# Optimization experiments

Measured on AMD Instinct MI355X. Metric: run time of the kernel, lower is better.

## Reference

```python
import jax, jax.numpy as jnp
import numpy as np

K = 7          # kernel_size
STRIDE = 1
GC = 4         # group_channels (fixed in module)
BN_EPS = 1e-5


def setup_inputs() -> dict:
    key = jax.random.key(0)
    ks = jax.random.split(key, 4)
    B, C, H, W = 4, 256, 56, 56
    Cr = C // 4              # reduction_ratio = 4
    G = C // GC              # groups = 64
    K2 = K * K               # 49
    x = jax.random.normal(ks[0], (B, C, H, W), jnp.float32)
    w1 = jax.random.normal(ks[1], (Cr, C), jnp.float32) * 0.05   # conv1 1x1
    b1 = jnp.zeros((Cr,), jnp.float32)
    gamma = jnp.ones((Cr,), jnp.float32)
    beta = jnp.zeros((Cr,), jnp.float32)
    bn_mean = jnp.zeros((Cr,), jnp.float32)
    bn_var = jnp.ones((Cr,), jnp.float32)
    w2 = jax.random.normal(ks[2], (K2 * G, Cr), jnp.float32) * 0.05  # conv2 1x1
    b2 = jnp.zeros((K2 * G,), jnp.float32)
    return {"x": x, "w1": w1, "b1": b1, "gamma": gamma, "beta": beta,
            "bn_mean": bn_mean, "bn_var": bn_var, "w2": w2, "b2": b2}


def reference(x, w1, b1, gamma, beta, bn_mean, bn_var, w2, b2):
    B, C, H, W = x.shape
    G = C // GC
    K2 = K * K
    p = (K - 1) // 2

    # kernel-generation branch (stride == 1 -> no avgpool)
    y = jnp.einsum('oc,bchw->bohw', w1, x) + b1[None, :, None, None]
    # BatchNorm (inference, running stats)
    inv = gamma / jnp.sqrt(bn_var + BN_EPS)
    y = y * inv[None, :, None, None] + (beta - bn_mean * inv)[None, :, None, None]
    y = jax.nn.relu(y)
    weight = jnp.einsum('oc,bchw->bohw', w2, y) + b2[None, :, None, None]
    Ho, Wo = weight.shape[2], weight.shape[3]
    weight = weight.reshape(B, G, K2, Ho, Wo)

    # unfold: zero-pad then gather k*k shifted views (channel-major like torch Unfold)
    xp = jnp.pad(x, ((0, 0), (0, 0), (p, p), (p, p)))
    patches = jnp.stack(
        [xp[:, :, i:i + H:STRIDE, j:j + W:STRIDE] for i in range(K) for j in range(K)],
        axis=2)                                    # (B, C, K2, Ho, Wo)
    patches = patches.reshape(B, G, GC, K2, Ho, Wo)

    # per-pixel dynamic kernel multiply-accumulate over k^2
    out = jnp.einsum('bgkhw,bgckhw->bgchw', weight, patches)
    return out.reshape(B, C, Ho, Wo)
```

## Files before the change

kernel.cpp:

```cpp
#include <hip/hip_runtime.h>
#include <hip/hip_fp16.h>

typedef _Float16 h8 __attribute__((ext_vector_type(8)));
typedef _Float16 h2v __attribute__((ext_vector_type(2)));
typedef __fp16 fp16x2 __attribute__((ext_vector_type(2)));
typedef float f32x4 __attribute__((ext_vector_type(4)));

#define HW 3136
#define NPX 12544
#define YSTR 96
#define XROW 14
#define XSEG 116
#define PS2 456
#define WGT_W 3648

union UH { unsigned int u; h2v h; fp16x2 p; };
__device__ __forceinline__ h2v uh(unsigned int u) { UH v; v.u = u; return v.h; }
__device__ __forceinline__ unsigned int hu(h2v h) { UH v; v.h = h; return v.u; }
#define BLO(w) __builtin_shufflevector(w, w, 0, 0)
#define BHI(w) __builtin_shufflevector(w, w, 1, 1)

__device__ __forceinline__ unsigned int pkrtz(float a, float b) {
    UH v; v.p = __builtin_amdgcn_cvt_pkrtz(a, b); return v.u;
}
__device__ __forceinline__ unsigned short f2hu(float f) {
    union { __half h; unsigned short u; } v; v.h = __float2half(f); return v.u;
}
__device__ __forceinline__ float fget(const float4& v, int e) {
    return e == 0 ? v.x : e == 1 ? v.y : e == 2 ? v.z : v.w;
}

__global__ __launch_bounds__(256) void kyw(
    const float* __restrict__ x, const float* __restrict__ w1,
    const float* __restrict__ b1, const float* __restrict__ gamma,
    const float* __restrict__ beta, const float* __restrict__ mean,
    const float* __restrict__ var, const float* __restrict__ w2,
    const float* __restrict__ b2, unsigned short* __restrict__ ytb,
    unsigned short* __restrict__ w2b96)
{
    __shared__ unsigned short xt[64 * 264];
    const int t = threadIdx.x, bid = blockIdx.x;

    if (bid >= 196) {
        const int r0 = (bid - 196) * 16;
#pragma unroll
        for (int i = 0; i < 6; ++i) {
            int j = i * 256 + t;
            int row = r0 + j / 96, col = j - (j / 96) * 96;
            int c8 = row / 448, rem = row - c8 * 448;
            int g = rem / 56, s = rem - g * 56;
            int ki = s >> 3, kj = s & 7;
            float v = 0.f;
            if (kj < 7) {
                int o = (c8 * 8 + g) * 49 + ki * 7 + kj;
                v = col < 64 ? w2[o * 64 + col] : (col == 64 ? b2[o] : 0.f);
            }
            w2b96[row * 96 + col] = f2hu(v);
        }
        return;
    }

    const int px0 = bid * 64;
    const int b = px0 / HW;
    const int p0 = px0 - b * HW;

    {
        unsigned int* xw = (unsigned int*)xt;
#pragma unroll
        for (int s = 0; s < 4; ++s)
#pragma unroll
            for (int i = 0; i < 2; ++i) {
                int j = i * 256 + t;
                int cp2 = j >> 2, pq = j & 3;
                const float* s0 = x + (size_t)(b * 256 + cp2 * 2) * HW
                                    + p0 + s * 16 + pq * 4;
                float4 v0 = *(const float4*)(s0);
                float4 v1 = *(const float4*)(s0 + HW);
                int pxb = s * 16 + pq * 4;
                xw[(pxb + 0) * 132 + cp2] = pkrtz(v0.x, v1.x);
                xw[(pxb + 1) * 132 + cp2] = pkrtz(v0.y, v1.y);
                xw[(pxb + 2) * 132 + cp2] = pkrtz(v0.z, v1.z);
                xw[(pxb + 3) * 132 + cp2] = pkrtz(v0.w, v1.w);
            }
    }
    if (t < 64) {
        unsigned short* yr = ytb + (size_t)(px0 + t) * YSTR + 64;
        ushort4 one; one.x = 0x3C00u; one.y = 0; one.z = 0; one.w = 0;
        ushort4 z; z.x = 0; z.y = 0; z.z = 0; z.w = 0;
        *(ushort4*)(yr) = one;
#pragma unroll
        for (int q = 1; q < 8; ++q) *(ushort4*)(yr + q * 4) = z;
    }
    __syncthreads();

    const int lane = t & 63, wave = t >> 6;
    const int n = lane & 15, quad = lane >> 4;
    const int m0 = wave * 16;

    h8 A[8];
#pragma unroll
    for (int k = 0; k < 8; ++k) {
        const float* wrow = w1 + (m0 + n) * 256 + k * 32 + quad * 8;
        float4 wa = *(const float4*)(wrow);
        float4 wb = *(const float4*)(wrow + 4);
        union { uint4 u; h8 h; } Au;
        Au.u.x = pkrtz(wa.x, wa.y);
        Au.u.y = pkrtz(wa.z, wa.w);
        Au.u.z = pkrtz(wb.x, wb.y);
        Au.u.w = pkrtz(wb.z, wb.w);
        A[k] = Au.h;
    }
    float sc[4], sh[4];
#pragma unroll
    for (int r = 0; r < 4; ++r) {
        int m = m0 + quad * 4 + r;
        sc[r] = gamma[m] * rsqrtf(var[m] + 1e-5f);
        sh[r] = beta[m] - mean[m] * sc[r] + b1[m] * sc[r];
    }

#pragma unroll
    for (int s = 0; s < 4; ++s) {
        f32x4 acc = {0.f, 0.f, 0.f, 0.f};
#pragma unroll
        for (int k = 0; k < 8; ++k) {
            h8 bv = *(const h8*)(&xt[(s * 16 + n) * 264 + k * 32 + quad * 8]);
            acc = __builtin_amdgcn_mfma_f32_16x16x32_f16(A[k], bv, acc, 0, 0, 0);
        }
        uint2 pk;
        pk.x = pkrtz(fmaxf(acc[0] * sc[0] + sh[0], 0.f),
                     fmaxf(acc[1] * sc[1] + sh[1], 0.f));
        pk.y = pkrtz(fmaxf(acc[2] * sc[2] + sh[2], 0.f),
                     fmaxf(acc[3] * sc[3] + sh[3], 0.f));
        *(uint2*)(ytb + (size_t)(px0 + s * 16 + n) * YSTR + m0 + quad * 4) = pk;
    }
}

__global__ __launch_bounds__(256, 7) void kmain(
    const float* __restrict__ x, const unsigned short* __restrict__ w2b96,
    const unsigned short* __restrict__ ytb, float* __restrict__ out)
{
    __shared__ __align__(16) unsigned int smem_u[WGT_W + 16 * XSEG];
    unsigned short* wgt16 = (unsigned short*)smem_u;
    unsigned int* xsb = smem_u + WGT_W;

    const int t = threadIdx.x;
    const int pix = t & 15, sub = t >> 4;
    const int lane = t & 63, wave = t >> 6;
    const int bc = blockIdx.x;
    const int b = bc >> 3, c8 = bc & 7;
    const int w0 = blockIdx.y * 8, h0 = blockIdx.z * 2;
    const int ph = pix >> 3, pw = pix & 7;
    const int h = h0 + ph, w = w0 + pw;
    const int n = lane & 15, quad = lane >> 4;

    const int Pn = b * HW + (h0 + (n >> 3)) * 56 + w0 + (n & 7);
    const unsigned short* yrp = ytb + (size_t)Pn * YSTR + quad * 8;
    const h8 bf0 = *(const h8*)(yrp);
    const h8 bf1 = *(const h8*)(yrp + 32);
    const h8 bf2 = *(const h8*)(yrp + 64);

    if (t < 128) {
        const int seg = t & 15, jr = t >> 4;
        const int jg = seg >> 1, jcp = seg & 1;
        const int hh = h0 + jr - 3;
        const bool rowok = (hh >= 0) && (hh < 56);
        const float* src = x + ((size_t)b * 256 + c8 * 32 + jg * 4 + jcp * 2) * HW + hh * 56;
        float4 va[2][4];
#pragma unroll
        for (int q = 0; q < 4; ++q) {
            int col0 = w0 - 4 + q * 4;
            bool ok = rowok && (col0 >= 0) && (col0 <= 52);
#pragma unroll
            for (int ci = 0; ci < 2; ++ci)
                va[ci][q] = ok ? *(const float4*)(src + ci * HW + col0)
                              : make_float4(0.f, 0.f, 0.f, 0.f);
        }
        unsigned int* dst = xsb + seg * XSEG + jr * XROW;
#pragma unroll
        for (int q = 0; q < 4; ++q)
#pragma unroll
            for (int e = 0; e < 4; ++e) {
                int c = q * 4 + e - 1;
                if (c >= 0 && c < 14)
                    dst[c] = pkrtz(fget(va[0][q], e), fget(va[1][q], e));
            }
    }

    {
        const int c0 = c8 * 448;
        for (int tile = wave; tile < 28; tile += 4) {
            const unsigned short* ap = w2b96 + (size_t)(c0 + tile * 16 + n) * 96 + quad * 8;
            h8 af0 = *(const h8*)(ap);
            h8 af1 = *(const h8*)(ap + 32);
            h8 af2 = *(const h8*)(ap + 64);
            f32x4 acc = {0.f, 0.f, 0.f, 0.f};
            acc = __builtin_amdgcn_mfma_f32_16x16x32_f16(af0, bf0, acc, 0, 0, 0);
            acc = __builtin_amdgcn_mfma_f32_16x16x32_f16(af1, bf1, acc, 0, 0, 0);
            acc = __builtin_amdgcn_mfma_f32_16x16x32_f16(af2, bf2, acc, 0, 0, 0);
            uint2 pk2;
            pk2.x = pkrtz(acc[0], acc[1]);
            pk2.y = pkrtz(acc[2], acc[3]);
            *(uint2*)(wgt16 + n * PS2 + tile * 16 + quad * 4) = pk2;
        }
    }
    __syncthreads();

    const int g = sub & 7, cp = sub >> 3;
    const unsigned short* wr16 = wgt16 + pix * PS2 + g * 56;
    const unsigned int* xr = xsb + (g * 2 + cp) * XSEG + ph * XROW + pw;
    h2v acA = {(_Float16)0.f, (_Float16)0.f};
    h2v acB = acA;
#pragma unroll
    for (int ki = 0; ki < 7; ++ki) {
        uint4 wq = *(const uint4*)(wr16 + ki * 8);
        const unsigned int* xrow = xr + ki * XROW;
        unsigned int xv[7];
#pragma unroll
        for (int j = 0; j < 7; ++j) xv[j] = xrow[j];
        h2v w01 = uh(wq.x), w23 = uh(wq.y), w45 = uh(wq.z), w6p = uh(wq.w);
        acA += BLO(w01) * uh(xv[0]);
        acB += BHI(w01) * uh(xv[1]);
        acA += BLO(w23) * uh(xv[2]);
        acB += BHI(w23) * uh(xv[3]);
        acA += BLO(w45) * uh(xv[4]);
        acB += BHI(w45) * uh(xv[5]);
        acA += BLO(w6p) * uh(xv[6]);
    }
    h2v acc2 = acA + acB;
    float a0 = (float)acc2[0];
    float a1 = (float)acc2[1];

    size_t ob = ((size_t)b * 256 + c8 * 32 + g * 4 + cp * 2) * HW + h * 56 + w;
    out[ob] = a0;
    out[ob + HW] = a1;
}

extern "C" void kernel_launch(void* const* d_in, const int* in_sizes, int n_in,
                              void* d_out, int out_size, void* d_ws, size_t ws_size,
                              hipStream_t stream) {
    const float* x     = (const float*)d_in[0];
    const float* w1    = (const float*)d_in[1];
    const float* b1    = (const float*)d_in[2];
    const float* gamma = (const float*)d_in[3];
    const float* beta  = (const float*)d_in[4];
    const float* mean  = (const float*)d_in[5];
    const float* var   = (const float*)d_in[6];
    const float* w2    = (const float*)d_in[7];
    const float* b2    = (const float*)d_in[8];
    float* out = (float*)d_out;

    unsigned short* ytb   = (unsigned short*)d_ws;
    unsigned short* w2b96 = ytb + (size_t)NPX * YSTR;
    hipLaunchKernelGGL(kyw, dim3(420), dim3(256), 0, stream,
                       x, w1, b1, gamma, beta, mean, var, w2, b2, ytb, w2b96);
    hipLaunchKernelGGL(kmain, dim3(32, 7, 28), dim3(256), 0, stream,
                       x, w2b96, ytb, out);
}
```

Baseline: 133.9 us.

## Process four output rows per block in kmain to reuse weight tiles and input halo

Each kmain block now covers a 4x8 pixel tile instead of 2x8, halving the grid along H. The w2 A-fragments loaded per tile feed two MFMA chains (for two 16-pixel groups), and the x halo (10 rows instead of 8) is staged once for both row pairs. The intent is to cut redundant w2 global loads and halo reloads. In exchange it doubles shared memory for generated weights, lowers occupancy to 4 blocks/SM, and raises register pressure.

Measured after the change: 121.7 us. 9.1% less time.

```diff
diff --git a/kernel.cpp b/kernel.cpp
--- a/kernel.cpp
+++ b/kernel.cpp
@@ -10,9 +10,9 @@
 #define NPX 12544
 #define YSTR 96
 #define XROW 14
-#define XSEG 116
+#define XSEG 148
 #define PS2 456
-#define WGT_W 3648
+#define WGT32_W 7296
 
 union UH { unsigned int u; h2v h; fp16x2 p; };
 __device__ __forceinline__ h2v uh(unsigned int u) { UH v; v.u = u; return v.h; }
@@ -135,31 +135,37 @@
     }
 }
 
-__global__ __launch_bounds__(256, 7) void kmain(
+__global__ __launch_bounds__(256, 4) void kmain(
     const float* __restrict__ x, const unsigned short* __restrict__ w2b96,
     const unsigned short* __restrict__ ytb, float* __restrict__ out)
 {
-    __shared__ __align__(16) unsigned int smem_u[WGT_W + 16 * XSEG];
+    __shared__ __align__(16) unsigned int smem_u[WGT32_W + 16 * XSEG];
     unsigned short* wgt16 = (unsigned short*)smem_u;
-    unsigned int* xsb = smem_u + WGT_W;
+    unsigned int* xsb = smem_u + WGT32_W;
 
     const int t = threadIdx.x;
     const int pix = t & 15, sub = t >> 4;
     const int lane = t & 63, wave = t >> 6;
     const int bc = blockIdx.x;
     const int b = bc >> 3, c8 = bc & 7;
-    const int w0 = blockIdx.y * 8, h0 = blockIdx.z * 2;
+    const int w0 = blockIdx.y * 8, h0 = blockIdx.z * 4;
     const int ph = pix >> 3, pw = pix & 7;
-    const int h = h0 + ph, w = w0 + pw;
     const int n = lane & 15, quad = lane >> 4;
 
-    const int Pn = b * HW + (h0 + (n >> 3)) * 56 + w0 + (n & 7);
-    const unsigned short* yrp = ytb + (size_t)Pn * YSTR + quad * 8;
-    const h8 bf0 = *(const h8*)(yrp);
-    const h8 bf1 = *(const h8*)(yrp + 32);
-    const h8 bf2 = *(const h8*)(yrp + 64);
-
-    if (t < 128) {
+    h8 bfa[3], bfb[3];
+    {
+        const int Pa = b * HW + (h0 + (n >> 3)) * 56 + w0 + (n & 7);
+        const unsigned short* ya = ytb + (size_t)Pa * YSTR + quad * 8;
+        bfa[0] = *(const h8*)(ya);
+        bfa[1] = *(const h8*)(ya + 32);
+        bfa[2] = *(const h8*)(ya + 64);
+        const unsigned short* yb = ya + (size_t)112 * YSTR;
+        bfb[0] = *(const h8*)(yb);
+        bfb[1] = *(const h8*)(yb + 32);
+        bfb[2] = *(const h8*)(yb + 64);
+    }
+
+    if (t < 160) {
         const int seg = t & 15, jr = t >> 4;
         const int jg = seg >> 1, jcp = seg & 1;
         const int hh = h0 + jr - 3;
@@ -193,46 +199,55 @@
             h8 af0 = *(const h8*)(ap);
             h8 af1 = *(const h8*)(ap + 32);
             h8 af2 = *(const h8*)(ap + 64);
-            f32x4 acc = {0.f, 0.f, 0.f, 0.f};
-            acc = __builtin_amdgcn_mfma_f32_16x16x32_f16(af0, bf0, acc, 0, 0, 0);
-            acc = __builtin_amdgcn_mfma_f32_16x16x32_f16(af1, bf1, acc, 0, 0, 0);
-            acc = __builtin_amdgcn_mfma_f32_16x16x32_f16(af2, bf2, acc, 0, 0, 0);
-            uint2 pk2;
-            pk2.x = pkrtz(acc[0], acc[1]);
-            pk2.y = pkrtz(acc[2], acc[3]);
-            *(uint2*)(wgt16 + n * PS2 + tile * 16 + quad * 4) = pk2;
+            f32x4 aca = {0.f, 0.f, 0.f, 0.f};
+            aca = __builtin_amdgcn_mfma_f32_16x16x32_f16(af0, bfa[0], aca, 0, 0, 0);
+            aca = __builtin_amdgcn_mfma_f32_16x16x32_f16(af1, bfa[1], aca, 0, 0, 0);
+            aca = __builtin_amdgcn_mfma_f32_16x16x32_f16(af2, bfa[2], aca, 0, 0, 0);
+            f32x4 acb = {0.f, 0.f, 0.f, 0.f};
+            acb = __builtin_amdgcn_mfma_f32_16x16x32_f16(af0, bfb[0], acb, 0, 0, 0);
+            acb = __builtin_amdgcn_mfma_f32_16x16x32_f16(af1, bfb[1], acb, 0, 0, 0);
+            acb = __builtin_amdgcn_mfma_f32_16x16x32_f16(af2, bfb[2], acb, 0, 0, 0);
+            uint2 pka, pkb;
+            pka.x = pkrtz(aca[0], aca[1]);
+            pka.y = pkrtz(aca[2], aca[3]);
+            pkb.x = pkrtz(acb[0], acb[1]);
+            pkb.y = pkrtz(acb[2], acb[3]);
+            *(uint2*)(wgt16 + n * PS2 + tile * 16 + quad * 4) = pka;
+            *(uint2*)(wgt16 + (16 + n) * PS2 + tile * 16 + quad * 4) = pkb;
         }
     }
     __syncthreads();
 
     const int g = sub & 7, cp = sub >> 3;
-    const unsigned short* wr16 = wgt16 + pix * PS2 + g * 56;
-    const unsigned int* xr = xsb + (g * 2 + cp) * XSEG + ph * XROW + pw;
-    h2v acA = {(_Float16)0.f, (_Float16)0.f};
-    h2v acB = acA;
-#pragma unroll
-    for (int ki = 0; ki < 7; ++ki) {
-        uint4 wq = *(const uint4*)(wr16 + ki * 8);
-        const unsigned int* xrow = xr + ki * XROW;
-        unsigned int xv[7];
-#pragma unroll
-        for (int j = 0; j < 7; ++j) xv[j] = xrow[j];
-        h2v w01 = uh(wq.x), w23 = uh(wq.y), w45 = uh(wq.z), w6p = uh(wq.w);
-        acA += BLO(w01) * uh(xv[0]);
-        acB += BHI(w01) * uh(xv[1]);
-        acA += BLO(w23) * uh(xv[2]);
-        acB += BHI(w23) * uh(xv[3]);
-        acA += BLO(w45) * uh(xv[4]);
-        acB += BHI(w45) * uh(xv[5]);
-        acA += BLO(w6p) * uh(xv[6]);
-    }
-    h2v acc2 = acA + acB;
-    float a0 = (float)acc2[0];
-    float a1 = (float)acc2[1];
-
-    size_t ob = ((size_t)b * 256 + c8 * 32 + g * 4 + cp * 2) * HW + h * 56 + w;
-    out[ob] = a0;
-    out[ob + HW] = a1;
+    const unsigned int* xrb = xsb + (g * 2 + cp) * XSEG + pw;
+#pragma unroll
+    for (int php = 0; php < 2; ++php) {
+        const unsigned short* wr16 = wgt16 + (php * 16 + pix) * PS2 + g * 56;
+        const unsigned int* xr = xrb + (php * 2 + ph) * XROW;
+        h2v acA = {(_Float16)0.f, (_Float16)0.f};
+        h2v acB = acA;
+#pragma unroll
+        for (int ki = 0; ki < 7; ++ki) {
+            uint4 wq = *(const uint4*)(wr16 + ki * 8);
+            const unsigned int* xrow = xr + ki * XROW;
+            unsigned int xv[7];
+#pragma unroll
+            for (int j = 0; j < 7; ++j) xv[j] = xrow[j];
+            h2v w01 = uh(wq.x), w23 = uh(wq.y), w45 = uh(wq.z), w6p = uh(wq.w);
+            acA += BLO(w01) * uh(xv[0]);
+            acB += BHI(w01) * uh(xv[1]);
+            acA += BLO(w23) * uh(xv[2]);
+            acB += BHI(w23) * uh(xv[3]);
+            acA += BLO(w45) * uh(xv[4]);
+            acB += BHI(w45) * uh(xv[5]);
+            acA += BLO(w6p) * uh(xv[6]);
+        }
+        h2v acc2 = acA + acB;
+        int h = h0 + php * 2 + ph;
+        size_t ob = ((size_t)b * 256 + c8 * 32 + g * 4 + cp * 2) * HW + h * 56 + w0 + pw;
+        out[ob] = (float)acc2[0];
+        out[ob + HW] = (float)acc2[1];
+    }
 }
 
 extern "C" void kernel_launch(void* const* d_in, const int* in_sizes, int n_in,
@@ -253,6 +268,6 @@
     unsigned short* w2b96 = ytb + (size_t)NPX * YSTR;
     hipLaunchKernelGGL(kyw, dim3(420), dim3(256), 0, stream,
                        x, w1, b1, gamma, beta, mean, var, w2, b2, ytb, w2b96);
-    hipLaunchKernelGGL(kmain, dim3(32, 7, 28), dim3(256), 0, stream,
+    hipLaunchKernelGGL(kmain, dim3(32, 7, 14), dim3(256), 0, stream,
                        x, w2b96, ytb, out);
 }
```
